# Kernel optimization log

Measured on AMD Instinct MI355X. Metric: run time of the kernel, lower is better.

## Reference

```python
import jax, jax.numpy as jnp
import numpy as np

N = 118784   # 1024 graphs * 116 ROIs
E = 3000000  # total edges
IN = 116     # node feature dim (correlation row)
EMB = 16     # group embedding dim
H = 64       # hidden_channels
ED = 5       # edge_dim
L = 3        # num_layers
OUT = 2
NG = N // 116  # number of graphs


def setup_inputs():
    key = jax.random.key(0)
    ks = jax.random.split(key, 16)

    def nrm(k, shape, scale):
        return jax.random.normal(k, shape, dtype=jnp.float32) * scale

    gw = (2.0 / (H + H)) ** 0.5
    inp = {
        'x': jax.random.normal(ks[0], (N, IN), dtype=jnp.float32),
        'edge_attr': jax.random.normal(ks[1], (E, ED), dtype=jnp.float32),
        'edge_index': jax.random.randint(ks[2], (2, E), 0, N),
        'batch_ids': jnp.arange(N) // 116,
        'group_ids': jnp.arange(N) % 8,
        'emb': nrm(ks[3], (8, EMB), 0.3),
        'W_enc': nrm(ks[4], (IN + EMB, H), (2.0 / (IN + EMB + H)) ** 0.5),
        'b_enc': jnp.zeros((H,), jnp.float32),
        'gamma_e': jnp.ones((H,), jnp.float32),
        'beta_e': jnp.zeros((H,), jnp.float32),
        'We0': nrm(ks[5], (ED, H), (2.0 / (ED + H)) ** 0.5),
        'be0': jnp.zeros((H,), jnp.float32),
        'W10': nrm(ks[6], (H, H), gw), 'b10': jnp.zeros((H,), jnp.float32),
        'W20': nrm(ks[7], (H, H), gw), 'b20': jnp.zeros((H,), jnp.float32),
        'We': nrm(ks[8], (L, ED, H), (2.0 / (ED + H)) ** 0.5),
        'be': jnp.zeros((L, H), jnp.float32),
        'W1': nrm(ks[9], (L, H, H), gw), 'b1': jnp.zeros((L, H), jnp.float32),
        'W2': nrm(ks[10], (L, H, H), gw), 'b2': jnp.zeros((L, H), jnp.float32),
        'gamma': jnp.ones((H,), jnp.float32),
        'beta': jnp.zeros((H,), jnp.float32),
        'Wl1': nrm(ks[11], (H, IN), (2.0 / (H + IN)) ** 0.5),
        'bl1': jnp.zeros((IN,), jnp.float32),
        'Wl2': nrm(ks[12], (IN, OUT), (2.0 / (IN + OUT)) ** 0.5),
        'bl2': jnp.zeros((OUT,), jnp.float32),
    }
    return inp


def _bn(h, g, b):
    # BatchNorm (training-mode batch stats), eps=1e-5
    m = jnp.mean(h, axis=0)
    v = jnp.var(h, axis=0)
    return g * (h - m) * jax.lax.rsqrt(v + 1e-5) + b


def _gine(h, src, dst, ea_lin, W1, b1, W2, b2):
    # GINEConv: msg = relu(x_j + lin_edge(e)); out = mlp((1+eps)*x + sum msg), eps=0
    m = jax.nn.relu(h[src] + ea_lin)                      # [E, H] gather + add
    agg = jax.ops.segment_sum(m, dst, num_segments=h.shape[0])  # scatter-add
    z = h + agg
    return jax.nn.relu(z @ W1 + b1) @ W2 + b2


def reference(x, edge_attr, edge_index, batch_ids, group_ids, emb, W_enc, b_enc,
              gamma_e, beta_e, We0, be0, W10, b10, W20, b20,
              We, be, W1, b1, W2, b2, gamma, beta, Wl1, bl1, Wl2, bl2):
    src, dst = edge_index[0], edge_index[1]
    # encode + embed (dropout = identity in eval)
    h = jnp.concatenate([x, emb[group_ids]], axis=-1)     # [N, IN+EMB]
    h = jax.nn.relu(h @ W_enc + b_enc)                    # [N, H]
    h = _bn(h, gamma_e, beta_e)
    h = jax.nn.relu(_gine(h, src, dst, edge_attr @ We0 + be0, W10, b10, W20, b20))
    # GINE stack
    for l in range(L):
        h = _gine(h, src, dst, edge_attr @ We[l] + be[l], W1[l], b1[l], W2[l], b2[l])
        h = jax.nn.relu(_bn(h, gamma, beta))
    # global_add_pool + head
    pooled = jax.ops.segment_sum(h, batch_ids, num_segments=NG)  # [NG, H]
    out = jax.nn.relu(pooled) @ Wl1 + bl1
    return out @ Wl2 + bl2
```

## Files before the change

kernel.cpp:

```cpp
#include <hip/hip_runtime.h>
#include <hip/hip_bf16.h>

typedef __hip_bfloat16 bf16;
typedef __attribute__((ext_vector_type(8))) short short8;
typedef __attribute__((ext_vector_type(4))) float floatx4;

#define NNODES 118784
#define NEDGES 3000000
#define INDIM 116
#define EMBD 16
#define HID 64
#define NGRAPH 1024
#define ROIS 116
#define NBINS 1024
#define BCAP 3456
#define CBLK 4096
#define NBLKC 733
#define NBLKC_PAD 736

__device__ __forceinline__ float b2f(bf16 v) { return __bfloat162float(v); }
__device__ __forceinline__ bf16 f2b(float v) { return __float2bfloat16(v); }
__device__ __forceinline__ unsigned f2u(float v) {
    bf16 b = __float2bfloat16(v);
    return (unsigned)*reinterpret_cast<unsigned short*>(&b);
}
__device__ __forceinline__ float uf(unsigned u) { return __uint_as_float(u); }

__global__ __launch_bounds__(256) void bincnt_kernel(
    const int* __restrict__ dst, int* __restrict__ cntMat)
{
    __shared__ int h[NBINS];
    for (int i = threadIdx.x; i < NBINS; i += 256) h[i] = 0;
    __syncthreads();
    const int base = blockIdx.x * CBLK;
    const int end = min(base + CBLK, NEDGES);
    for (int i = base + threadIdx.x; i < end; i += 256)
        atomicAdd(&h[(unsigned)dst[i] / 116u], 1);
    __syncthreads();
    for (int i = threadIdx.x; i < NBINS; i += 256)
        cntMat[i * NBLKC_PAD + blockIdx.x] = h[i];
}

__global__ __launch_bounds__(256) void colscan_kernel(
    int* __restrict__ cntMat, int* __restrict__ binCnt)
{
    __shared__ int sd[256];
    int* row = cntMat + blockIdx.x * NBLKC_PAD;
    const int t = threadIdx.x;
    int v[3]; int s = 0;
    #pragma unroll
    for (int j = 0; j < 3; j++) {
        const int idx = t * 3 + j;
        v[j] = (idx < NBLKC) ? row[idx] : 0;
        s += v[j];
    }
    sd[t] = s;
    __syncthreads();
    for (int d = 1; d < 256; d <<= 1) {
        int x = (t >= d) ? sd[t - d] : 0;
        __syncthreads();
        sd[t] += x;
        __syncthreads();
    }
    int ex = (t == 0) ? 0 : sd[t - 1];
    #pragma unroll
    for (int j = 0; j < 3; j++) {
        const int idx = t * 3 + j;
        if (idx < NBLKC) { const int val = v[j]; row[idx] = ex; ex += val; }
    }
    if (t == 255) binCnt[blockIdx.x] = ex;
}

__global__ __launch_bounds__(256) void binscan_kernel(
    const int* __restrict__ binCnt, int* __restrict__ binOff,
    int* __restrict__ offN)
{
    __shared__ int sd[256];
    const int t = threadIdx.x;
    int c[4]; int s = 0;
    #pragma unroll
    for (int j = 0; j < 4; j++) { c[j] = binCnt[t * 4 + j]; s += c[j]; }
    sd[t] = s;
    __syncthreads();
    for (int d = 1; d < 256; d <<= 1) {
        int v = (t >= d) ? sd[t - d] : 0;
        __syncthreads();
        sd[t] += v;
        __syncthreads();
    }
    int ex = (t == 0) ? 0 : sd[t - 1];
    #pragma unroll
    for (int j = 0; j < 4; j++) { binOff[t * 4 + j] = ex; ex += c[j]; }
    if (t == 0) { binOff[NBINS] = NEDGES; offN[0] = NEDGES; }
}

__global__ __launch_bounds__(256) void binplace_kernel(
    const int* __restrict__ src, const int* __restrict__ dst,
    const float* __restrict__ ea, const int* __restrict__ posMat,
    const int* __restrict__ binOff, uint4* __restrict__ rec)
{
    __shared__ int cursor[NBINS];
    const int blk = blockIdx.x;
    for (int i = threadIdx.x; i < NBINS; i += 256)
        cursor[i] = posMat[i * NBLKC_PAD + blk] + binOff[i];
    __syncthreads();
    const int base = blk * CBLK;
    const int end = min(base + CBLK, NEDGES);
    for (int e = base + threadIdx.x; e < end; e += 256) {
        const unsigned d = (unsigned)dst[e];
        const unsigned bin = d / 116u;
        const unsigned dl = d - bin * 116u;
        const float* a = ea + (size_t)e * 5;
        const unsigned m0 = f2u(a[0]) | (f2u(a[1]) << 16);
        const unsigned m1 = f2u(a[2]) | (f2u(a[3]) << 16);
        const unsigned m2 = f2u(a[4]);
        const int p = atomicAdd(&cursor[bin], 1);
        rec[p] = make_uint4((unsigned)src[e] | (dl << 20), m0, m1, m2);
    }
}

__global__ __launch_bounds__(256) void binsort_kernel(
    uint4* __restrict__ rec, const int* __restrict__ binOff,
    int* __restrict__ off)
{
    __shared__ uint4 buf[BCAP];
    __shared__ int cnt[128];
    __shared__ int sc[128];
    const int b = blockIdx.x, t = threadIdx.x;
    const int n0 = binOff[b];
    const int n  = binOff[b + 1] - n0;
    if (t < 128) cnt[t] = 0;
    __syncthreads();
    for (int i = t; i < n; i += 256) {
        uint4 r = rec[n0 + i];
        buf[i] = r;
        atomicAdd(&cnt[r.x >> 20], 1);
    }
    __syncthreads();
    if (t < 128) sc[t] = cnt[t];
    __syncthreads();
    for (int d = 1; d < 128; d <<= 1) {
        int v = 0;
        if (t < 128 && t >= d) v = sc[t - d];
        __syncthreads();
        if (t < 128) sc[t] += v;
        __syncthreads();
    }
    if (t < 116) {
        const int ex = sc[t] - cnt[t];
        off[b * 116 + t] = n0 + ex;
        cnt[t] = ex;
    }
    __syncthreads();
    for (int i = t; i < n; i += 256) {
        uint4 r = buf[i];
        const int p = atomicAdd(&cnt[r.x >> 20], 1);
        r.x = (r.x & 0xFFFFFu) << 7;
        rec[n0 + p] = r;
    }
}

__global__ __launch_bounds__(256) void pack_kernel(
    const float* __restrict__ Wenc,
    const float* __restrict__ W10, const float* __restrict__ W20,
    const float* __restrict__ W1, const float* __restrict__ W2,
    unsigned short* __restrict__ WPenc, unsigned short* __restrict__ WPh)
{
    const int b = blockIdx.x, tid = threadIdx.x;
    if (b == 0) {
        for (int i = tid; i < 10240; i += 256) {
            const int j = i & 7, lane = (i >> 3) & 63, t = i >> 9;
            const int c = t / 5, s = t - c * 5;
            const int k = s * 32 + (lane >> 4) * 8 + j;
            const int n = c * 16 + (lane & 15);
            const float v = (k < 132) ? Wenc[k * 64 + n] : 0.f;
            WPenc[i] = (unsigned short)f2u(v);
        }
        return;
    }
    const float* src = nullptr;
    unsigned short* dst = nullptr;
    switch (b) {
        case 1: src = W10;       dst = WPh + 0 * 4096; break;
        case 2: src = W20;       dst = WPh + 1 * 4096; break;
        case 3: src = W1;        dst = WPh + 2 * 4096; break;
        case 4: src = W2;        dst = WPh + 3 * 4096; break;
        case 5: src = W1 + 4096; dst = WPh + 4 * 4096; break;
        case 6: src = W2 + 4096; dst = WPh + 5 * 4096; break;
        case 7: src = W1 + 8192; dst = WPh + 6 * 4096; break;
        case 8: src = W2 + 8192; dst = WPh + 7 * 4096; break;
    }
    for (int i = tid; i < 4096; i += 256) {
        const int j = i & 7, lane = (i >> 3) & 63, t = i >> 9;
        const int c = t >> 1, s = t & 1;
        const int k = s * 32 + (lane >> 4) * 8 + j;
        const int n = c * 16 + (lane & 15);
        dst[i] = (unsigned short)f2u(src[k * 64 + n]);
    }
}

__global__ __launch_bounds__(256) void enc_kernel(
    const float* __restrict__ x, const int* __restrict__ gid,
    const float* __restrict__ emb, const unsigned short* __restrict__ WP,
    const float* __restrict__ benc,
    bf16* __restrict__ hb, float* __restrict__ stats)
{
    __shared__ float sred[4][128];

    const int tid  = threadIdx.x;
    const int lane = tid & 63;
    const int wv   = tid >> 6;
    const int m    = lane & 15;
    const int q    = lane >> 4;
    const int r0   = blockIdx.x * 64;

    const int arow = r0 + wv * 16 + m;
    const float* xr = x + (size_t)arow * INDIM;
    const float* er = emb + gid[arow] * EMBD;

    floatx4 acc[4];
    #pragma unroll
    for (int c = 0; c < 4; c++) acc[c] = {0.f, 0.f, 0.f, 0.f};

    #pragma unroll
    for (int s = 0; s < 5; s++) {
        float4 a, b;
        if (s < 3) {
            a = *(const float4*)(xr + s * 32 + q * 8);
            b = *(const float4*)(xr + s * 32 + q * 8 + 4);
        } else if (s == 3) {
            if (q < 2) {
                a = *(const float4*)(xr + 96 + q * 8);
                b = *(const float4*)(xr + 100 + q * 8);
            } else if (q == 2) {
                a = *(const float4*)(xr + 112);
                b = *(const float4*)(er);
            } else {
                a = *(const float4*)(er + 4);
                b = *(const float4*)(er + 8);
            }
        } else {
            if (q == 0) {
                a = *(const float4*)(er + 12);
                b = make_float4(0.f, 0.f, 0.f, 0.f);
            } else {
                a = make_float4(0.f, 0.f, 0.f, 0.f);
                b = a;
            }
        }
        short8 af;
        af[0] = (short)f2u(a.x); af[1] = (short)f2u(a.y);
        af[2] = (short)f2u(a.z); af[3] = (short)f2u(a.w);
        af[4] = (short)f2u(b.x); af[5] = (short)f2u(b.y);
        af[6] = (short)f2u(b.z); af[7] = (short)f2u(b.w);
        #pragma unroll
        for (int c = 0; c < 4; c++) {
            short8 bfr = *(const short8*)(WP + (size_t)(((c * 5 + s) * 64) + lane) * 8);
            acc[c] = __builtin_amdgcn_mfma_f32_16x16x32_bf16(af, bfr, acc[c], 0, 0, 0);
        }
    }

    #pragma unroll
    for (int c = 0; c < 4; c++) {
        const int ch = c * 16 + m;
        const float bb = benc[ch];
        float sv = 0.f, sq = 0.f;
        #pragma unroll
        for (int r = 0; r < 4; r++) {
            const int orow = r0 + wv * 16 + q * 4 + r;
            float a = fmaxf(acc[c][r] + bb, 0.f);
            hb[(size_t)orow * HID + ch] = f2b(a);
            sv += a; sq += a * a;
        }
        sv += __shfl_xor(sv, 16); sv += __shfl_xor(sv, 32);
        sq += __shfl_xor(sq, 16); sq += __shfl_xor(sq, 32);
        if (q == 0) { sred[wv][ch] = sv; sred[wv][64 + ch] = sq; }
    }
    __syncthreads();
    if (tid < 128) {
        const float s = sred[0][tid] + sred[1][tid] + sred[2][tid] + sred[3][tid];
        unsafeAtomicAdd(&stats[tid], s);
    }
}

template <int MODE>
__global__ __launch_bounds__(256) void agg_kernel(
    const bf16* __restrict__ hin, bf16* __restrict__ zout,
    const uint4* __restrict__ rec, const int* __restrict__ off,
    const float* __restrict__ We, const float* __restrict__ be,
    const float* __restrict__ stats, const float* __restrict__ gamma,
    const float* __restrict__ beta)
{
    const int lane = threadIdx.x & 63;
    const int node = blockIdx.x * 4 + __builtin_amdgcn_readfirstlane(threadIdx.x >> 6);
    if (node >= NNODES) return;

    float gg = 1.f, bbt = 0.f;
    if (MODE != 0) {
        const float m = stats[lane] * (1.f / NNODES);
        const float var = stats[64 + lane] * (1.f / NNODES) - m * m;
        const float inv = rsqrtf(var + 1e-5f);
        gg = gamma[lane] * inv;
        bbt = beta[lane] - gg * m;
    }
    const float w0 = We[lane], w1 = We[64 + lane], w2 = We[128 + lane];
    const float w3 = We[192 + lane], w4 = We[256 + lane];
    const float bel = be[lane];

    const int s0 = off[node];
    const int s1 = off[node + 1];

    const char* hlane = (const char*)hin + (lane << 1);

    float self = b2f(hin[(size_t)node * HID + lane]);
    if (MODE == 1) self = gg * self + bbt;
    if (MODE == 2) self = fmaxf(gg * self + bbt, 0.f);

    float acc = 0.f;
    int i = s0;

#define EDGE_TERM(R, HF)                                                     \
    {                                                                        \
        float hh = (HF);                                                     \
        if (MODE == 1) hh = gg * hh + bbt;                                   \
        if (MODE == 2) hh = fmaxf(gg * hh + bbt, 0.f);                       \
        const float v = bel                                                  \
            + uf((R).y << 16) * w0 + uf((R).y & 0xFFFF0000u) * w1            \
            + uf((R).z << 16) * w2 + uf((R).z & 0xFFFF0000u) * w3            \
            + uf((R).w << 16) * w4 + hh;                                     \
        acc += fmaxf(v, 0.f);                                                \
    }

    for (; i + 8 <= s1; i += 8) {
        uint4 r[8];
        #pragma unroll
        for (int j = 0; j < 8; j++) r[j] = rec[i + j];
        float h[8];
        #pragma unroll
        for (int j = 0; j < 8; j++)
            h[j] = uf((unsigned)*(const unsigned short*)(hlane + r[j].x) << 16);
        #pragma unroll
        for (int j = 0; j < 8; j++) EDGE_TERM(r[j], h[j])
    }
    for (; i + 4 <= s1; i += 4) {
        uint4 r[4];
        #pragma unroll
        for (int j = 0; j < 4; j++) r[j] = rec[i + j];
        float h[4];
        #pragma unroll
        for (int j = 0; j < 4; j++)
            h[j] = uf((unsigned)*(const unsigned short*)(hlane + r[j].x) << 16);
        #pragma unroll
        for (int j = 0; j < 4; j++) EDGE_TERM(r[j], h[j])
    }
    for (; i < s1; i++) {
        const uint4 r = rec[i];
        const float hf = uf((unsigned)*(const unsigned short*)(hlane + r.x) << 16);
        EDGE_TERM(r, hf)
    }
#undef EDGE_TERM

    zout[(size_t)node * HID + lane] = f2b(self + acc);
}

template <int MODE>
__global__ __launch_bounds__(256) void mlp_kernel(
    bf16* __restrict__ Zg,
    const unsigned short* __restrict__ W1P, const float* __restrict__ b1,
    const unsigned short* __restrict__ W2P, const float* __restrict__ b2,
    float* __restrict__ stats)
{
    __shared__ unsigned short Zl[64 * 72];
    __shared__ unsigned short Tl[64 * 72];
    __shared__ float sred[4][128];

    const int tid = threadIdx.x;
    const int r0 = blockIdx.x * 64;

    {
        const uint4* zg = (const uint4*)(Zg + (size_t)r0 * HID);
        for (int i = tid; i < 512; i += 256) {
            int row = i >> 3, ch = i & 7;
            *(uint4*)&Zl[row * 72 + ch * 8] = zg[row * 8 + ch];
        }
    }
    __syncthreads();

    const int lane = tid & 63;
    const int wv   = tid >> 6;
    const int m    = lane & 15;
    const int q    = lane >> 4;
    const int mrow = wv * 16;

    float bias1[4], bias2[4];
    #pragma unroll
    for (int c = 0; c < 4; c++) {
        bias1[c] = b1[c * 16 + m];
        bias2[c] = b2[c * 16 + m];
    }

    floatx4 acc[4];
    #pragma unroll
    for (int c = 0; c < 4; c++) acc[c] = {0.f, 0.f, 0.f, 0.f};
    #pragma unroll
    for (int s = 0; s < 2; s++) {
        short8 af = *(const short8*)&Zl[(mrow + m) * 72 + s * 32 + q * 8];
        #pragma unroll
        for (int c = 0; c < 4; c++) {
            short8 bfr = *(const short8*)(W1P + (size_t)(((c * 2 + s) * 64) + lane) * 8);
            acc[c] = __builtin_amdgcn_mfma_f32_16x16x32_bf16(af, bfr, acc[c], 0, 0, 0);
        }
    }
    #pragma unroll
    for (int c = 0; c < 4; c++)
        #pragma unroll
        for (int r = 0; r < 4; r++)
            Tl[(mrow + q * 4 + r) * 72 + c * 16 + m] =
                (unsigned short)f2u(fmaxf(acc[c][r] + bias1[c], 0.f));
    __syncthreads();

    #pragma unroll
    for (int c = 0; c < 4; c++) acc[c] = {0.f, 0.f, 0.f, 0.f};
    #pragma unroll
    for (int s = 0; s < 2; s++) {
        short8 af = *(const short8*)&Tl[(mrow + m) * 72 + s * 32 + q * 8];
        #pragma unroll
        for (int c = 0; c < 4; c++) {
            short8 bfr = *(const short8*)(W2P + (size_t)(((c * 2 + s) * 64) + lane) * 8);
            acc[c] = __builtin_amdgcn_mfma_f32_16x16x32_bf16(af, bfr, acc[c], 0, 0, 0);
        }
    }
    #pragma unroll
    for (int c = 0; c < 4; c++) {
        float sv = 0.f, sq = 0.f;
        #pragma unroll
        for (int r = 0; r < 4; r++) {
            float o = acc[c][r] + bias2[c];
            if (MODE == 0) o = fmaxf(o, 0.f);
            Zg[(size_t)(r0 + mrow + q * 4 + r) * HID + c * 16 + m] = f2b(o);
            if (MODE == 1) { sv += o; sq += o * o; }
        }
        if (MODE == 1) {
            sv += __shfl_xor(sv, 16); sv += __shfl_xor(sv, 32);
            sq += __shfl_xor(sq, 16); sq += __shfl_xor(sq, 32);
            if (q == 0) { sred[wv][c * 16 + m] = sv; sred[wv][64 + c * 16 + m] = sq; }
        }
    }
    if (MODE == 1) {
        __syncthreads();
        if (tid < 128) {
            const float s = sred[0][tid] + sred[1][tid] + sred[2][tid] + sred[3][tid];
            unsafeAtomicAdd(&stats[tid], s);
        }
    }
}

__global__ __launch_bounds__(128) void head_kernel(
    const bf16* __restrict__ hb, const float* __restrict__ Wl1,
    const float* __restrict__ bl1, const float* __restrict__ Wl2,
    const float* __restrict__ bl2, float* __restrict__ out,
    const float* __restrict__ stats, const float* __restrict__ gamma,
    const float* __restrict__ beta)
{
    __shared__ float part[2 * HID];
    __shared__ float ps[HID];
    __shared__ float r0[128], r1[128];

    const int g = blockIdx.x;
    const int tid = threadIdx.x;
    const int lane = tid & 63;
    const int wv = tid >> 6;
    const bf16* hbg = hb + (size_t)g * ROIS * HID;

    const float mm = stats[lane] * (1.f / NNODES);
    const float var = stats[64 + lane] * (1.f / NNODES) - mm * mm;
    const float inv = rsqrtf(var + 1e-5f);
    const float gg = gamma[lane] * inv;
    const float bbt = beta[lane] - gg * mm;

    float acc = 0.f;
    for (int r = wv; r < ROIS; r += 2)
        acc += fmaxf(gg * b2f(hbg[r * HID + lane]) + bbt, 0.f);
    part[wv * HID + lane] = acc;
    __syncthreads();
    if (tid < HID) ps[tid] = fmaxf(part[tid] + part[HID + tid], 0.f);
    __syncthreads();

    float e0 = 0.f, e1 = 0.f;
    if (tid < ROIS) {
        float a = bl1[tid];
        #pragma unroll 8
        for (int c = 0; c < HID; c++)
            a += ps[c] * Wl1[c * ROIS + tid];
        e0 = a * Wl2[tid * 2 + 0];
        e1 = a * Wl2[tid * 2 + 1];
    }
    r0[tid] = e0;
    r1[tid] = e1;
    __syncthreads();
    for (int s = 64; s > 0; s >>= 1) {
        if (tid < s) { r0[tid] += r0[tid + s]; r1[tid] += r1[tid + s]; }
        __syncthreads();
    }
    if (tid == 0) {
        out[g * 2 + 0] = r0[0] + bl2[0];
        out[g * 2 + 1] = r1[0] + bl2[1];
    }
}

extern "C" void kernel_launch(void* const* d_in, const int* in_sizes, int n_in,
                              void* d_out, int out_size, void* d_ws, size_t ws_size,
                              hipStream_t stream)
{
    const float* x       = (const float*)d_in[0];
    const float* ea      = (const float*)d_in[1];
    const int*   eidx    = (const int*)  d_in[2];
    const int*   gid     = (const int*)  d_in[4];
    const float* emb     = (const float*)d_in[5];
    const float* Wenc    = (const float*)d_in[6];
    const float* benc    = (const float*)d_in[7];
    const float* gamma_e = (const float*)d_in[8];
    const float* beta_e  = (const float*)d_in[9];
    const float* We0     = (const float*)d_in[10];
    const float* be0     = (const float*)d_in[11];
    const float* W10     = (const float*)d_in[12];
    const float* b10     = (const float*)d_in[13];
    const float* W20     = (const float*)d_in[14];
    const float* b20     = (const float*)d_in[15];
    const float* We      = (const float*)d_in[16];
    const float* be      = (const float*)d_in[17];
    const float* W1      = (const float*)d_in[18];
    const float* b1      = (const float*)d_in[19];
    const float* W2      = (const float*)d_in[20];
    const float* b2      = (const float*)d_in[21];
    const float* gamma   = (const float*)d_in[22];
    const float* beta    = (const float*)d_in[23];
    const float* Wl1     = (const float*)d_in[24];
    const float* bl1     = (const float*)d_in[25];
    const float* Wl2     = (const float*)d_in[26];
    const float* bl2     = (const float*)d_in[27];

    const int* srcp = eidx;
    const int* dstp = eidx + NEDGES;

    const size_t NH = (size_t)NNODES * HID;
    char* p = (char*)d_ws;
    bf16*  Abuf = (bf16*)p;  p += NH * 2;
    bf16*  Zbuf = (bf16*)p;  p += NH * 2;
    uint4* rec  = (uint4*)p; p += (size_t)NEDGES * 16;
    int* off    = (int*)p;   p += (size_t)(NNODES + 16) * 4;
    int* binCnt = (int*)p;   p += (NBINS + 16) * 4;
    int* binOff = (int*)p;   p += (NBINS + 16) * 4;
    int* cntMat = (int*)p;   p += (size_t)NBINS * NBLKC_PAD * 4;
    float* stats = (float*)p; p += 512 * 4;
    unsigned short* WPenc = (unsigned short*)p; p += 10240 * 2;
    unsigned short* WPh   = (unsigned short*)p; p += 8 * 4096 * 2;

    hipMemsetAsync(stats, 0, 512 * 4, stream);

    const int nb = NNODES / 4;

    pack_kernel<<<9, 256, 0, stream>>>(Wenc, W10, W20, W1, W2, WPenc, WPh);

    bincnt_kernel<<<NBLKC, 256, 0, stream>>>(dstp, cntMat);
    colscan_kernel<<<NBINS, 256, 0, stream>>>(cntMat, binCnt);
    binscan_kernel<<<1, 256, 0, stream>>>(binCnt, binOff, off + NNODES);
    binplace_kernel<<<NBLKC, 256, 0, stream>>>(srcp, dstp, ea, cntMat, binOff, rec);
    binsort_kernel<<<NBINS, 256, 0, stream>>>(rec, binOff, off);

    enc_kernel<<<NNODES / 64, 256, 0, stream>>>(x, gid, emb, WPenc, benc, Abuf, stats);

    agg_kernel<1><<<nb, 256, 0, stream>>>(Abuf, Zbuf, rec, off, We0, be0,
                                          stats, gamma_e, beta_e);
    mlp_kernel<0><<<NNODES / 64, 256, 0, stream>>>(Zbuf, WPh + 0 * 4096, b10,
                                                   WPh + 1 * 4096, b20, nullptr);

    agg_kernel<0><<<nb, 256, 0, stream>>>(Zbuf, Abuf, rec, off, We, be,
                                          nullptr, nullptr, nullptr);
    mlp_kernel<1><<<NNODES / 64, 256, 0, stream>>>(Abuf, WPh + 2 * 4096, b1,
                                                   WPh + 3 * 4096, b2, stats + 128);

    agg_kernel<2><<<nb, 256, 0, stream>>>(Abuf, Zbuf, rec, off,
                                          We + 320, be + 64,
                                          stats + 128, gamma, beta);
    mlp_kernel<1><<<NNODES / 64, 256, 0, stream>>>(Zbuf, WPh + 4 * 4096, b1 + 64,
                                                   WPh + 5 * 4096, b2 + 64, stats + 256);

    agg_kernel<2><<<nb, 256, 0, stream>>>(Zbuf, Abuf, rec, off,
                                          We + 640, be + 128,
                                          stats + 256, gamma, beta);
    mlp_kernel<1><<<NNODES / 64, 256, 0, stream>>>(Abuf, WPh + 6 * 4096, b1 + 128,
                                                   WPh + 7 * 4096, b2 + 128, stats + 384);

    head_kernel<<<NGRAPH, 128, 0, stream>>>(Abuf, Wl1, bl1, Wl2, bl2,
                                            (float*)d_out, stats + 384, gamma, beta);
}
```

Before: 869.3 us.

## Fuse edge aggregation and node MLP into one GINE kernel per layer

Merges the per-node aggregation kernel and the two-layer MFMA MLP kernel into a single kernel. Each wave aggregates 16 consecutive nodes in turn, writing the results straight into shared memory, then runs the MLP on those wave-local rows. This removes one launch per layer, the global write and re-read of the intermediate Z buffer, and one block barrier. In exchange, each wave handles nodes one after another, so there are far fewer independent waves in flight and less latency hiding for the gather. Uneven node degrees within a wave's 16 nodes may also leave waves idle.

```diff
diff --git a/kernel.cpp b/kernel.cpp
--- a/kernel.cpp
+++ b/kernel.cpp
@@ -283,47 +283,58 @@
     }
 }
 
-template <int MODE>
-__global__ __launch_bounds__(256) void agg_kernel(
+template <int AMODE, int MMODE>
+__global__ __launch_bounds__(256) void gine_kernel(
     const bf16* __restrict__ hin, bf16* __restrict__ zout,
     const uint4* __restrict__ rec, const int* __restrict__ off,
     const float* __restrict__ We, const float* __restrict__ be,
-    const float* __restrict__ stats, const float* __restrict__ gamma,
-    const float* __restrict__ beta)
-{
-    const int lane = threadIdx.x & 63;
-    const int node = blockIdx.x * 4 + __builtin_amdgcn_readfirstlane(threadIdx.x >> 6);
-    if (node >= NNODES) return;
-
-    float gg = 1.f, bbt = 0.f;
-    if (MODE != 0) {
-        const float m = stats[lane] * (1.f / NNODES);
-        const float var = stats[64 + lane] * (1.f / NNODES) - m * m;
-        const float inv = rsqrtf(var + 1e-5f);
-        gg = gamma[lane] * inv;
-        bbt = beta[lane] - gg * m;
-    }
-    const float w0 = We[lane], w1 = We[64 + lane], w2 = We[128 + lane];
-    const float w3 = We[192 + lane], w4 = We[256 + lane];
-    const float bel = be[lane];
-
-    const int s0 = off[node];
-    const int s1 = off[node + 1];
-
-    const char* hlane = (const char*)hin + (lane << 1);
-
-    float self = b2f(hin[(size_t)node * HID + lane]);
-    if (MODE == 1) self = gg * self + bbt;
-    if (MODE == 2) self = fmaxf(gg * self + bbt, 0.f);
-
-    float acc = 0.f;
-    int i = s0;
+    const float* __restrict__ statsIn, const float* __restrict__ gamma,
+    const float* __restrict__ beta,
+    const unsigned short* __restrict__ W1P, const float* __restrict__ b1,
+    const unsigned short* __restrict__ W2P, const float* __restrict__ b2,
+    float* __restrict__ statsOut)
+{
+    __shared__ unsigned short Zl[64 * 72];
+    __shared__ unsigned short Tl[64 * 72];
+    __shared__ float sred[4][128];
+
+    const int tid  = threadIdx.x;
+    const int lane = tid & 63;
+    const int wv   = __builtin_amdgcn_readfirstlane(tid >> 6);
+    const int r0   = blockIdx.x * 64;
+
+    {
+        float gg = 1.f, bbt = 0.f;
+        if (AMODE != 0) {
+            const float m = statsIn[lane] * (1.f / NNODES);
+            const float var = statsIn[64 + lane] * (1.f / NNODES) - m * m;
+            const float inv = rsqrtf(var + 1e-5f);
+            gg = gamma[lane] * inv;
+            bbt = beta[lane] - gg * m;
+        }
+        const float w0 = We[lane], w1 = We[64 + lane], w2 = We[128 + lane];
+        const float w3 = We[192 + lane], w4 = We[256 + lane];
+        const float bel = be[lane];
+
+        const char* hlane = (const char*)hin + (lane << 1);
+
+        for (int t = 0; t < 16; t++) {
+            const int node = r0 + wv * 16 + t;
+            const int s0 = off[node];
+            const int s1 = off[node + 1];
+
+            float self = b2f(hin[(size_t)node * HID + lane]);
+            if (AMODE == 1) self = gg * self + bbt;
+            if (AMODE == 2) self = fmaxf(gg * self + bbt, 0.f);
+
+            float acc = 0.f;
+            int i = s0;
 
 #define EDGE_TERM(R, HF)                                                     \
     {                                                                        \
         float hh = (HF);                                                     \
-        if (MODE == 1) hh = gg * hh + bbt;                                   \
-        if (MODE == 2) hh = fmaxf(gg * hh + bbt, 0.f);                       \
+        if (AMODE == 1) hh = gg * hh + bbt;                                  \
+        if (AMODE == 2) hh = fmaxf(gg * hh + bbt, 0.f);                      \
         const float v = bel                                                  \
             + uf((R).y << 16) * w0 + uf((R).y & 0xFFFF0000u) * w1            \
             + uf((R).z << 16) * w2 + uf((R).z & 0xFFFF0000u) * w3            \
@@ -331,63 +342,39 @@
         acc += fmaxf(v, 0.f);                                                \
     }
 
-    for (; i + 8 <= s1; i += 8) {
-        uint4 r[8];
-        #pragma unroll
-        for (int j = 0; j < 8; j++) r[j] = rec[i + j];
-        float h[8];
-        #pragma unroll
-        for (int j = 0; j < 8; j++)
-            h[j] = uf((unsigned)*(const unsigned short*)(hlane + r[j].x) << 16);
-        #pragma unroll
-        for (int j = 0; j < 8; j++) EDGE_TERM(r[j], h[j])
-    }
-    for (; i + 4 <= s1; i += 4) {
-        uint4 r[4];
-        #pragma unroll
-        for (int j = 0; j < 4; j++) r[j] = rec[i + j];
-        float h[4];
-        #pragma unroll
-        for (int j = 0; j < 4; j++)
-            h[j] = uf((unsigned)*(const unsigned short*)(hlane + r[j].x) << 16);
-        #pragma unroll
-        for (int j = 0; j < 4; j++) EDGE_TERM(r[j], h[j])
-    }
-    for (; i < s1; i++) {
-        const uint4 r = rec[i];
-        const float hf = uf((unsigned)*(const unsigned short*)(hlane + r.x) << 16);
-        EDGE_TERM(r, hf)
-    }
+            for (; i + 8 <= s1; i += 8) {
+                uint4 r[8];
+                #pragma unroll
+                for (int j = 0; j < 8; j++) r[j] = rec[i + j];
+                float h[8];
+                #pragma unroll
+                for (int j = 0; j < 8; j++)
+                    h[j] = uf((unsigned)*(const unsigned short*)(hlane + r[j].x) << 16);
+                #pragma unroll
+                for (int j = 0; j < 8; j++) EDGE_TERM(r[j], h[j])
+            }
+            for (; i + 4 <= s1; i += 4) {
+                uint4 r[4];
+                #pragma unroll
+                for (int j = 0; j < 4; j++) r[j] = rec[i + j];
+                float h[4];
+                #pragma unroll
+                for (int j = 0; j < 4; j++)
+                    h[j] = uf((unsigned)*(const unsigned short*)(hlane + r[j].x) << 16);
+                #pragma unroll
+                for (int j = 0; j < 4; j++) EDGE_TERM(r[j], h[j])
+            }
+            for (; i < s1; i++) {
+                const uint4 r = rec[i];
+                const float hf = uf((unsigned)*(const unsigned short*)(hlane + r.x) << 16);
+                EDGE_TERM(r, hf)
+            }
 #undef EDGE_TERM
 
-    zout[(size_t)node * HID + lane] = f2b(self + acc);
-}
-
-template <int MODE>
-__global__ __launch_bounds__(256) void mlp_kernel(
-    bf16* __restrict__ Zg,
-    const unsigned short* __restrict__ W1P, const float* __restrict__ b1,
-    const unsigned short* __restrict__ W2P, const float* __restrict__ b2,
-    float* __restrict__ stats)
-{
-    __shared__ unsigned short Zl[64 * 72];
-    __shared__ unsigned short Tl[64 * 72];
-    __shared__ float sred[4][128];
-
-    const int tid = threadIdx.x;
-    const int r0 = blockIdx.x * 64;
-
-    {
-        const uint4* zg = (const uint4*)(Zg + (size_t)r0 * HID);
-        for (int i = tid; i < 512; i += 256) {
-            int row = i >> 3, ch = i & 7;
-            *(uint4*)&Zl[row * 72 + ch * 8] = zg[row * 8 + ch];
-        }
-    }
-    __syncthreads();
-
-    const int lane = tid & 63;
-    const int wv   = tid >> 6;
+            Zl[(wv * 16 + t) * 72 + lane] = (unsigned short)f2u(self + acc);
+        }
+    }
+
     const int m    = lane & 15;
     const int q    = lane >> 4;
     const int mrow = wv * 16;
@@ -417,7 +404,6 @@
         for (int r = 0; r < 4; r++)
             Tl[(mrow + q * 4 + r) * 72 + c * 16 + m] =
                 (unsigned short)f2u(fmaxf(acc[c][r] + bias1[c], 0.f));
-    __syncthreads();
 
     #pragma unroll
     for (int c = 0; c < 4; c++) acc[c] = {0.f, 0.f, 0.f, 0.f};
@@ -436,21 +422,21 @@
         #pragma unroll
         for (int r = 0; r < 4; r++) {
             float o = acc[c][r] + bias2[c];
-            if (MODE == 0) o = fmaxf(o, 0.f);
-            Zg[(size_t)(r0 + mrow + q * 4 + r) * HID + c * 16 + m] = f2b(o);
-            if (MODE == 1) { sv += o; sq += o * o; }
-        }
-        if (MODE == 1) {
+            if (MMODE == 0) o = fmaxf(o, 0.f);
+            zout[(size_t)(r0 + mrow + q * 4 + r) * HID + c * 16 + m] = f2b(o);
+            if (MMODE == 1) { sv += o; sq += o * o; }
+        }
+        if (MMODE == 1) {
             sv += __shfl_xor(sv, 16); sv += __shfl_xor(sv, 32);
             sq += __shfl_xor(sq, 16); sq += __shfl_xor(sq, 32);
             if (q == 0) { sred[wv][c * 16 + m] = sv; sred[wv][64 + c * 16 + m] = sq; }
         }
     }
-    if (MODE == 1) {
+    if (MMODE == 1) {
         __syncthreads();
         if (tid < 128) {
             const float s = sred[0][tid] + sred[1][tid] + sred[2][tid] + sred[3][tid];
-            unsafeAtomicAdd(&stats[tid], s);
+            unsafeAtomicAdd(&statsOut[tid], s);
         }
     }
 }
@@ -558,7 +544,7 @@
 
     hipMemsetAsync(stats, 0, 512 * 4, stream);
 
-    const int nb = NNODES / 4;
+    const int gb = NNODES / 64;
 
     pack_kernel<<<9, 256, 0, stream>>>(Wenc, W10, W20, W1, W2, WPenc, WPh);
 
@@ -570,27 +556,21 @@
 
     enc_kernel<<<NNODES / 64, 256, 0, stream>>>(x, gid, emb, WPenc, benc, Abuf, stats);
 
-    agg_kernel<1><<<nb, 256, 0, stream>>>(Abuf, Zbuf, rec, off, We0, be0,
-                                          stats, gamma_e, beta_e);
-    mlp_kernel<0><<<NNODES / 64, 256, 0, stream>>>(Zbuf, WPh + 0 * 4096, b10,
-                                                   WPh + 1 * 4096, b20, nullptr);
-
-    agg_kernel<0><<<nb, 256, 0, stream>>>(Zbuf, Abuf, rec, off, We, be,
-                                          nullptr, nullptr, nullptr);
-    mlp_kernel<1><<<NNODES / 64, 256, 0, stream>>>(Abuf, WPh + 2 * 4096, b1,
-                                                   WPh + 3 * 4096, b2, stats + 128);
-
-    agg_kernel<2><<<nb, 256, 0, stream>>>(Abuf, Zbuf, rec, off,
-                                          We + 320, be + 64,
-                                          stats + 128, gamma, beta);
-    mlp_kernel<1><<<NNODES / 64, 256, 0, stream>>>(Zbuf, WPh + 4 * 4096, b1 + 64,
-                                                   WPh + 5 * 4096, b2 + 64, stats + 256);
-
-    agg_kernel<2><<<nb, 256, 0, stream>>>(Zbuf, Abuf, rec, off,
-                                          We + 640, be + 128,
-                                          stats + 256, gamma, beta);
-    mlp_kernel<1><<<NNODES / 64, 256, 0, stream>>>(Abuf, WPh + 6 * 4096, b1 + 128,
-                                                   WPh + 7 * 4096, b2 + 128, stats + 384);
+    gine_kernel<1, 0><<<gb, 256, 0, stream>>>(
+        Abuf, Zbuf, rec, off, We0, be0, stats, gamma_e, beta_e,
+        WPh + 0 * 4096, b10, WPh + 1 * 4096, b20, nullptr);
+
+    gine_kernel<0, 1><<<gb, 256, 0, stream>>>(
+        Zbuf, Abuf, rec, off, We, be, nullptr, nullptr, nullptr,
+        WPh + 2 * 4096, b1, WPh + 3 * 4096, b2, stats + 128);
+
+    gine_kernel<2, 1><<<gb, 256, 0, stream>>>(
+        Abuf, Zbuf, rec, off, We + 320, be + 64, stats + 128, gamma, beta,
+        WPh + 4 * 4096, b1 + 64, WPh + 5 * 4096, b2 + 64, stats + 256);
+
+    gine_kernel<2, 1><<<gb, 256, 0, stream>>>(
+        Zbuf, Abuf, rec, off, We + 640, be + 128, stats + 256, gamma, beta,
+        WPh + 6 * 4096, b1 + 128, WPh + 7 * 4096, b2 + 128, stats + 384);
 
     head_kernel<<<NGRAPH, 128, 0, stream>>>(Abuf, Wl1, bl1, Wl2, bl2,
                                             (float*)d_out, stats + 384, gamma, beta);
```

Result: slower. 900.7 us (+3.6%).
